# Performance work log

Measured on AMD Instinct MI355X. Metric: run time of the kernel, lower is better.

Reference implementation:

```python
import jax, jax.numpy as jnp
import numpy as np

N, E, H, ED, TD = 10000, 320000, 128, 64, 32

def _lin(x, w, b):
    return x @ w + b

def _ln(x, g, b, eps=1e-5):
    m = jnp.mean(x, axis=-1, keepdims=True)
    v = jnp.var(x, axis=-1, keepdims=True)
    return (x - m) * jax.lax.rsqrt(v + eps) * g + b

def _mlp(x, w1, b1, g, bt, w2, b2):
    y = jax.nn.silu(_ln(_lin(x, w1, b1), g, bt))
    return _lin(y, w2, b2)

def setup_inputs() -> dict:
    key = jax.random.key(0)
    ks = jax.random.split(key, 32)
    s = 0.02
    nrm = lambda k, shp: jax.random.normal(k, shp, jnp.float32) * s
    d = {}
    d['h'] = jax.random.normal(ks[0], (N, H), jnp.float32)
    d['edge_attr'] = jax.random.normal(ks[1], (E, ED), jnp.float32)
    d['edge_time_emb'] = jax.random.normal(ks[2], (E, TD), jnp.float32)
    d['edge_index'] = jax.random.randint(ks[3], (2, E), 0, N)
    # edge_emb + edge_norm
    d['w_ee'] = nrm(ks[4], (ED + TD, ED)); d['b_ee'] = jnp.zeros((ED,), jnp.float32)
    d['g_en'] = jnp.ones((ED + TD,), jnp.float32); d['bt_en'] = jnp.zeros((ED + TD,), jnp.float32)
    # node_linear / bond_linear
    d['w_nl'] = nrm(ks[5], (H, H)); d['b_nl'] = jnp.zeros((H,), jnp.float32)
    d['w_bl'] = nrm(ks[6], (ED, H)); d['b_bl'] = jnp.zeros((H,), jnp.float32)
    # bond_linear_left/right, node_linear_left/right
    d['w_bll'] = nrm(ks[7], (ED, H)); d['b_bll'] = jnp.zeros((H,), jnp.float32)
    d['w_blr'] = nrm(ks[8], (ED, H)); d['b_blr'] = jnp.zeros((H,), jnp.float32)
    d['w_nll'] = nrm(ks[9], (H, H)); d['b_nll'] = jnp.zeros((H,), jnp.float32)
    d['w_nlr'] = nrm(ks[10], (H, H)); d['b_nlr'] = jnp.zeros((H,), jnp.float32)
    # left / right MLPs: Linear(2H,H), LayerNorm(H), SiLU, Linear(H,H)
    d['mlpl_w1'] = nrm(ks[11], (2 * H, H)); d['mlpl_b1'] = jnp.zeros((H,), jnp.float32)
    d['mlpl_g'] = jnp.ones((H,), jnp.float32); d['mlpl_bt'] = jnp.zeros((H,), jnp.float32)
    d['mlpl_w2'] = nrm(ks[12], (H, H)); d['mlpl_b2'] = jnp.zeros((H,), jnp.float32)
    d['mlpr_w1'] = nrm(ks[13], (2 * H, H)); d['mlpr_b1'] = jnp.zeros((H,), jnp.float32)
    d['mlpr_g'] = jnp.ones((H,), jnp.float32); d['mlpr_bt'] = jnp.zeros((H,), jnp.float32)
    d['mlpr_w2'] = nrm(ks[14], (H, H)); d['mlpr_b2'] = jnp.zeros((H,), jnp.float32)
    # layer_norm(3H) + bond_out: Linear(3H,H), SiLU, Linear(H,ED)
    d['g_ln'] = jnp.ones((3 * H,), jnp.float32); d['bt_ln'] = jnp.zeros((3 * H,), jnp.float32)
    d['w_o1'] = nrm(ks[15], (3 * H, H)); d['b_o1'] = jnp.zeros((H,), jnp.float32)
    d['w_o2'] = nrm(ks[16], (H, ED)); d['b_o2'] = jnp.zeros((ED,), jnp.float32)
    return d

def reference(h, edge_attr, edge_time_emb, edge_index,
              w_ee, b_ee, g_en, bt_en, w_nl, b_nl, w_bl, b_bl,
              w_bll, b_bll, w_blr, b_blr, w_nll, b_nll, w_nlr, b_nlr,
              mlpl_w1, mlpl_b1, mlpl_g, mlpl_bt, mlpl_w2, mlpl_b2,
              mlpr_w1, mlpr_b1, mlpr_g, mlpr_bt, mlpr_w2, mlpr_b2,
              g_ln, bt_ln, w_o1, b_o1, w_o2, b_o2):
    src, dst = edge_index[0], edge_index[1]
    n = h.shape[0]
    # edge_attr = edge_emb(edge_norm(cat([edge_attr, edge_time_emb])))
    ea = _lin(_ln(jnp.concatenate([edge_attr, edge_time_emb], axis=-1), g_en, bt_en), w_ee, b_ee)
    # node linears applied per-node then gathered (same math as gather-then-linear)
    x_i = _lin(h, w_nll, b_nll)[src]            # [E, H]
    x_j = _lin(h, w_nlr, b_nlr)[dst]            # [E, H]
    edge_i = _lin(ea, w_bll, b_bll)             # [E, H]
    edge_j = _lin(ea, w_blr, b_blr)             # [E, H]
    inter_i = _mlp(jnp.concatenate([edge_i, x_i], axis=-1), mlpl_w1, mlpl_b1, mlpl_g, mlpl_bt, mlpl_w2, mlpl_b2)
    inter_j = _mlp(jnp.concatenate([edge_j, x_j], axis=-1), mlpr_w1, mlpr_b1, mlpr_g, mlpr_bt, mlpr_w2, mlpr_b2)
    # scatter_sum to nodes, then regather on the same index
    inter_i = jax.ops.segment_sum(inter_i, src, num_segments=n)[src]
    inter_j = jax.ops.segment_sum(inter_j, dst, num_segments=n)[dst]
    h_node = _lin(h, w_nl, b_nl)
    h_bond = jnp.concatenate([inter_i + inter_j, h_node[src] + h_node[dst], _lin(ea, w_bl, b_bl)], axis=-1)  # [E, 3H]
    h_bond = _ln(h_bond, g_ln, bt_ln)
    out = _lin(jax.nn.silu(_lin(h_bond, w_o1, b_o1)), w_o2, b_o2)  # [E, ED]
    return out
```

## Files before the change

kernel.cpp:

```cpp
#include <hip/hip_runtime.h>
#include <math.h>


using u16 = unsigned short;
using u32 = unsigned int;
typedef __attribute__((ext_vector_type(8))) short  short8;
typedef __attribute__((ext_vector_type(4))) float  f32x4;
typedef __attribute__((ext_vector_type(4))) u32    uint4v;
typedef __attribute__((ext_vector_type(2))) u32    uint2v;

constexpr int NN = 10000;
constexpr int EE = 320000;
constexpr int MAXDEG = 96;

__device__ __forceinline__ float b2f(u16 v) {
  return __builtin_bit_cast(float, (u32)v << 16);
}
__device__ __forceinline__ float b2f_lo(u32 v) {
  return __builtin_bit_cast(float, v << 16);
}
__device__ __forceinline__ float b2f_hi(u32 v) {
  return __builtin_bit_cast(float, v & 0xffff0000u);
}
__device__ __forceinline__ u32 cvtpk(float lo, float hi) {
  u32 r;
  asm("v_cvt_pk_bf16_f32 %0, %1, %2" : "=v"(r) : "v"(lo), "v"(hi));
  return r;
}
__device__ __forceinline__ u16 f2b(float f) {
  return (u16)cvtpk(f, f);
}
__device__ __forceinline__ uint2v pack4(f32x4 v) {
  uint2v r;
  r.x = cvtpk(v[0], v[1]);
  r.y = cvtpk(v[2], v[3]);
  return r;
}
__device__ __forceinline__ u32 addpk(u32 a, u32 b) {
  return cvtpk(b2f_lo(a) + b2f_lo(b), b2f_hi(a) + b2f_hi(b));
}
__device__ __forceinline__ float silu_f(float v) {
  return v * __builtin_amdgcn_rcpf(1.f + __expf(-v));
}
template<typename T>
__device__ __forceinline__ T ntld(const T* p) { return __builtin_nontemporal_load(p); }
template<typename T>
__device__ __forceinline__ void ntst(T* p, T v) { __builtin_nontemporal_store(v, p); }

struct Params {
  const void* h; const void* edge_attr; const void* te;
  const int* eidx;
  const int* flag;
  const u16 *b_ee, *g_en, *bt_en;
  const u16 *b_nl, *b_bl, *b_bll, *b_blr, *b_nll, *b_nlr;
  const u16 *l_b1, *l_g, *l_bt, *l_b2;
  const u16 *r_b1, *r_g, *r_bt, *r_b2;
  const u16 *g_ln, *bt_ln, *b_o1, *b_o2;
  const u16 *w_eeT, *w_blT, *w_bllT, *w_blrT, *w_nlT, *w_nllT, *w_nlrT;
  const u16 *l_w1T, *l_w2T, *r_w1T, *r_w2T, *o1T, *o2T;
  u16 *a_nll, *a_nlr, *tbl_i, *ea_ws;
  u32 *cnt0, *cnt1, *elist0, *elist1;
  u16 *accb_j;
  float *accf_i, *accf_j;
  u16 *inter0, *inter1;
  int amode;
  void *out;
};

__global__ __launch_bounds__(256) void k_sniff(const u16* p, int* flag)
{
  __shared__ int c;
  if (threadIdx.x == 0) c = 0;
  __syncthreads();
  u16 v = p[threadIdx.x * 2];
  int e = (v >> 7) & 0xff;
  if (e >= 100 && e <= 140) atomicAdd(&c, 1);
  __syncthreads();
  if (threadIdx.x == 0) *flag = (c >= 200) ? 1 : 0;
}

template<int K, int CT, int RT>
__device__ __forceinline__ void wave_gemm(const u16* A, int SA,
                                          const u16* __restrict__ BT,
                                          f32x4 (&acc)[RT][CT], int n0)
{
  const int lane = threadIdx.x & 63;
  const int quad = lane >> 4, l16 = lane & 15;
  constexpr int NKT = K / 32;
  constexpr int G = NKT < 4 ? NKT : 4;
#pragma unroll
  for (int g0 = 0; g0 < NKT; g0 += G) {
    short8 b[G][CT];
#pragma unroll
    for (int gg = 0; gg < G; ++gg)
#pragma unroll
      for (int c = 0; c < CT; ++c)
        b[gg][c] = *(const short8*)(BT + (size_t)(n0 + c * 16 + l16) * K +
                                    (g0 + gg) * 32 + quad * 8);
    __builtin_amdgcn_sched_barrier(0);
#pragma unroll
    for (int gg = 0; gg < G; ++gg) {
      const int k0 = (g0 + gg) * 32 + quad * 8;
#pragma unroll
      for (int rt = 0; rt < RT; ++rt) {
        short8 av = *(const short8*)(A + (rt * 16 + l16) * SA + k0);
#pragma unroll
        for (int c = 0; c < CT; ++c)
          acc[rt][c] = __builtin_amdgcn_mfma_f32_16x16x32_bf16(av, b[gg][c], acc[rt][c], 0, 0, 0);
      }
    }
  }
}

template<int CT, int RT, bool SILU>
__device__ __forceinline__ void epi_lds(f32x4 (&acc)[RT][CT], u16* O, int SO,
                                        int outc0, const u16* __restrict__ bias,
                                        int biasc0)
{
  const int lane = threadIdx.x & 63;
  const int quad = lane >> 4, l16 = lane & 15;
#pragma unroll
  for (int c = 0; c < CT; ++c) {
    float bv = b2f(bias[biasc0 + c * 16 + l16]);
#pragma unroll
    for (int rt = 0; rt < RT; ++rt) {
#pragma unroll
      for (int r = 0; r < 4; ++r) {
        float v = acc[rt][c][r] + bv;
        if (SILU) v = silu_f(v);
        O[(rt * 16 + quad * 4 + r) * SO + outc0 + c * 16 + l16] = f2b(v);
      }
    }
  }
}

template<int D, int ROWS, bool SILU>
__device__ __forceinline__ void ln_rows(u16* buf, int S,
                                        const u16* __restrict__ g,
                                        const u16* __restrict__ bt, float* red)
{
  constexpr int P = 256 / ROWS;
  constexpr int C = D / P;
  constexpr int NV = C / 8;
  const int t = threadIdx.x;
  const int row = t / P, p = t % P;
  u16* r = buf + row * S + p * C;
  uint4v vv[NV];
  float s = 0.f, ss = 0.f;
#pragma unroll
  for (int n = 0; n < NV; ++n) {
    vv[n] = *(const uint4v*)(r + n * 8);
#pragma unroll
    for (int q = 0; q < 4; ++q) {
      float lo = b2f_lo(vv[n][q]), hi = b2f_hi(vv[n][q]);
      s += lo + hi;
      ss += lo * lo + hi * hi;
    }
  }
  red[row * 2 * P + p] = s;
  red[row * 2 * P + P + p] = ss;
  __syncthreads();
  float S1 = 0.f, S2 = 0.f;
#pragma unroll
  for (int q = 0; q < P / 4; ++q) {
    f32x4 x = *(const f32x4*)&red[row * 2 * P + q * 4];
    f32x4 y = *(const f32x4*)&red[row * 2 * P + P + q * 4];
    S1 += x[0] + x[1] + x[2] + x[3];
    S2 += y[0] + y[1] + y[2] + y[3];
  }
  const float mean = S1 / (float)D;
  const float var  = S2 / (float)D - mean * mean;
  const float rstd = rsqrtf(var + 1e-5f);
#pragma unroll
  for (int n = 0; n < NV; ++n) {
    uint4v gv = *(const uint4v*)(g + p * C + n * 8);
    uint4v bv = *(const uint4v*)(bt + p * C + n * 8);
    uint4v ov;
#pragma unroll
    for (int q = 0; q < 4; ++q) {
      float lo = (b2f_lo(vv[n][q]) - mean) * rstd * b2f_lo(gv[q]) + b2f_lo(bv[q]);
      float hi = (b2f_hi(vv[n][q]) - mean) * rstd * b2f_hi(gv[q]) + b2f_hi(bv[q]);
      if (SILU) { lo = silu_f(lo); hi = silu_f(hi); }
      ov[q] = cvtpk(lo, hi);
    }
    *(uint4v*)(r + n * 8) = ov;
  }
  __syncthreads();
}

struct TDesc { const void* s; u16* d; int K; int N; };
struct TArgs { TDesc t[34]; const int* flag; };

__global__ __launch_bounds__(256) void k_transpose(TArgs a)
{
  const int flag = *a.flag;
  TDesc dsc = a.t[blockIdx.y];
  const int total = dsc.K * dsc.N;
  for (int i = blockIdx.x * 256 + threadIdx.x; i < total; i += gridDim.x * 256) {
    int n = i / dsc.K;
    int k = i - n * dsc.K;
    size_t si = (size_t)k * dsc.N + n;
    dsc.d[i] = flag ? ((const u16*)dsc.s)[si] : f2b(((const float*)dsc.s)[si]);
  }
}

__global__ __launch_bounds__(256) void k_hist(const int* eidx, u32* cnt0,
                                              u32* elist0, u32* cnt1, u32* elist1)
{
  int e = blockIdx.x * 256 + threadIdx.x;
  if (e >= EE) return;
  int n0 = eidx[e];
  u32 p0 = atomicAdd(&cnt0[n0], 1u);
  if (p0 < MAXDEG) elist0[(size_t)n0 * MAXDEG + p0] = (u32)e;
  int n1 = eidx[EE + e];
  u32 p1 = atomicAdd(&cnt1[n1], 1u);
  if (p1 < MAXDEG) elist1[(size_t)n1 * MAXDEG + p1] = (u32)e;
}

__global__ __launch_bounds__(256) void k_node(Params a)
{
  __shared__ __align__(16) u16 hs[64 * 136];
  const int tid = threadIdx.x, w = tid >> 6;
  const int n0 = blockIdx.x * 64;
  const int flag = *a.flag;
  if (flag) {
    for (int c = tid; c < 1024; c += 256) {
      int row = c >> 4, cc = c & 15;
      int node = n0 + row;
      uint4v v = {};
      if (node < NN) v = ntld((const uint4v*)((const u16*)a.h + (size_t)node * 128 + cc * 8));
      *(uint4v*)&hs[row * 136 + cc * 8] = v;
    }
  } else {
    for (int c = tid; c < 2048; c += 256) {
      int row = c >> 5, cc = c & 31;
      int node = n0 + row;
      uint2v pk = {};
      if (node < NN) {
        f32x4 fv = ntld((const f32x4*)((const float*)a.h + (size_t)node * 128 + cc * 4));
        pk = pack4(fv);
      }
      *(uint2v*)&hs[row * 136 + cc * 4] = pk;
    }
  }
  __syncthreads();
  const u16* wT[3] = { a.w_nllT, a.w_nlrT, a.w_nlT };
  const u16* bs[3] = { a.b_nll, a.b_nlr, a.b_nl };
  u16* os[3] = { a.a_nll, a.a_nlr, a.tbl_i + 128 };
  const int st[3] = { 128, 128, 256 };
  const int lane = tid & 63, quad = lane >> 4, l16 = lane & 15;
#pragma unroll 1
  for (int m = 0; m < 3; ++m) {
    f32x4 acc[4][2] = {};
    wave_gemm<128, 2, 4>(hs, 136, wT[m], acc, w * 32);
#pragma unroll
    for (int c = 0; c < 2; ++c) {
      int col = w * 32 + c * 16 + l16;
      float bv = b2f(bs[m][col]);
#pragma unroll
      for (int rt = 0; rt < 4; ++rt) {
#pragma unroll
        for (int r = 0; r < 4; ++r) {
          int node = n0 + rt * 16 + quad * 4 + r;
          if (node < NN) os[m][(size_t)node * st[m] + col] = f2b(acc[rt][c][r] + bv);
        }
      }
    }
  }
}

__global__ __launch_bounds__(256) void k_ea(Params a)
{
  __shared__ __align__(16) u16 u[64 * 104];
  __shared__ __align__(16) u16 eas[64 * 72];
  __shared__ float red[512];
  const int tid = threadIdx.x, w = tid >> 6;
  const int e0 = blockIdx.x * 64;
  const int flag = *a.flag;
  if (flag) {
    for (int c = tid; c < 512; c += 256) {
      int row = c >> 3, cc = c & 7;
      *(uint4v*)&u[row * 104 + cc * 8] =
          ntld((const uint4v*)((const u16*)a.edge_attr + (size_t)(e0 + row) * 64 + cc * 8));
    }
    {
      int row = tid >> 2, cc = tid & 3;
      *(uint4v*)&u[row * 104 + 64 + cc * 8] =
          ntld((const uint4v*)((const u16*)a.te + (size_t)(e0 + row) * 32 + cc * 8));
    }
  } else {
    for (int c = tid; c < 1024; c += 256) {
      int row = c >> 4, cc = c & 15;
      f32x4 fv = ntld((const f32x4*)((const float*)a.edge_attr + (size_t)(e0 + row) * 64 + cc * 4));
      *(uint2v*)&u[row * 104 + cc * 4] = pack4(fv);
    }
    for (int c = tid; c < 512; c += 256) {
      int row = c >> 3, cc = c & 7;
      f32x4 fv = ntld((const f32x4*)((const float*)a.te + (size_t)(e0 + row) * 32 + cc * 4));
      *(uint2v*)&u[row * 104 + 64 + cc * 4] = pack4(fv);
    }
  }
  __syncthreads();
  ln_rows<96, 64, false>(u, 104, a.g_en, a.bt_en, red);
  {
    f32x4 acc[4][1] = {};
    wave_gemm<96, 1, 4>(u, 104, a.w_eeT, acc, w * 16);
    epi_lds<1, 4, false>(acc, eas, 72, w * 16, a.b_ee, w * 16);
  }
  __syncthreads();
  for (int c = tid; c < 512; c += 256) {
    int row = c >> 3, cc = c & 7;
    *(uint4v*)(a.ea_ws + (size_t)(e0 + row) * 64 + cc * 8) =
        *(const uint4v*)&eas[row * 72 + cc * 8];
  }
}

template<bool ATOMIC>
__global__ __launch_bounds__(256, 4) void k_mlp(
    const u16* __restrict__ ea_ws, const int* __restrict__ eidx_side,
    const u16* __restrict__ an, const u16* __restrict__ wbT,
    const u16* __restrict__ bb, const u16* __restrict__ w1T,
    const u16* __restrict__ b1, const u16* __restrict__ gg,
    const u16* __restrict__ bt, const u16* __restrict__ w2T,
    const u16* __restrict__ b2, u16* __restrict__ inter,
    float* __restrict__ accf)
{
  __shared__ __align__(16) u16 u[64 * 264];
  __shared__ float red[512];
  __shared__ int sidx[64];
  const int tid = threadIdx.x, w = tid >> 6;
  const int e0 = blockIdx.x * 64;
  const int lane = tid & 63, quad = lane >> 4, l16 = lane & 15;

  if (tid < 64) sidx[tid] = eidx_side[e0 + tid];
  __syncthreads();
  for (int c = tid; c < 1024; c += 256) {
    int row = c >> 4, cc = c & 15;
    *(uint4v*)&u[row * 264 + 128 + cc * 8] =
        *(const uint4v*)(an + (size_t)sidx[row] * 128 + cc * 8);
  }
  {
    f32x4 acc[4][2] = {};
    wave_gemm<64, 2, 4>(ea_ws + (size_t)e0 * 64, 64, wbT, acc, w * 32);
    epi_lds<2, 4, false>(acc, u, 264, w * 32, bb, w * 32);
  }
  __syncthreads();
  {
    f32x4 acc[4][2] = {};
    wave_gemm<256, 2, 4>(u, 264, w1T, acc, w * 32);
    __syncthreads();
    epi_lds<2, 4, false>(acc, u, 264, w * 32, b1, w * 32);
  }
  __syncthreads();
  ln_rows<128, 64, true>(u, 264, gg, bt, red);
  {
    f32x4 acc[4][2] = {};
    wave_gemm<128, 2, 4>(u, 264, w2T, acc, w * 32);
    if (ATOMIC) {
#pragma unroll
      for (int c = 0; c < 2; ++c) {
        int col = w * 32 + c * 16 + l16;
        float bias = b2f(b2[col]);
#pragma unroll
        for (int rt = 0; rt < 4; ++rt)
#pragma unroll
          for (int r = 0; r < 4; ++r) {
            int row = rt * 16 + quad * 4 + r;
            unsafeAtomicAdd(accf + (size_t)sidx[row] * 128 + col,
                            acc[rt][c][r] + bias);
          }
      }
    } else {
      epi_lds<2, 4, false>(acc, u, 264, 128 + w * 32, b2, w * 32);
      __syncthreads();
      for (int c = tid; c < 1024; c += 256) {
        int row = c >> 4, cc = c & 15;
        ntst((uint4v*)(inter + (size_t)(e0 + row) * 128 + cc * 8),
             *(const uint4v*)&u[row * 264 + 128 + cc * 8]);
      }
    }
  }
}

__global__ __launch_bounds__(256) void k_nodesum(const u16* __restrict__ inter,
                                                 const u32* __restrict__ cnt,
                                                 const u32* __restrict__ elist,
                                                 u16* __restrict__ dst, int dstride)
{
  const int wv = (blockIdx.x * 256 + threadIdx.x) >> 6;
  const int lane = threadIdx.x & 63;
  if (wv >= NN) return;
  u32 deg = cnt[wv];
  if (deg > MAXDEG) deg = MAXDEG;
  const u32* el = elist + (size_t)wv * MAXDEG;
  float s0 = 0.f, s1 = 0.f;
  u32 d = 0;
  for (; d + 4 <= deg; d += 4) {
    uint4v ev = ntld((const uint4v*)(el + d));
    u32 v0 = ntld((const u32*)(inter + (size_t)ev[0] * 128 + lane * 2));
    u32 v1 = ntld((const u32*)(inter + (size_t)ev[1] * 128 + lane * 2));
    u32 v2 = ntld((const u32*)(inter + (size_t)ev[2] * 128 + lane * 2));
    u32 v3 = ntld((const u32*)(inter + (size_t)ev[3] * 128 + lane * 2));
    s0 += b2f_lo(v0) + b2f_lo(v1) + b2f_lo(v2) + b2f_lo(v3);
    s1 += b2f_hi(v0) + b2f_hi(v1) + b2f_hi(v2) + b2f_hi(v3);
  }
  for (; d < deg; ++d) {
    u32 e = el[d];
    u32 v = ntld((const u32*)(inter + (size_t)e * 128 + lane * 2));
    s0 += b2f_lo(v);
    s1 += b2f_hi(v);
  }
  *(u32*)(dst + (size_t)wv * dstride + lane * 2) = cvtpk(s0, s1);
}

__global__ __launch_bounds__(256, 4) void k_stage2(Params a)
{
  __shared__ __align__(16) u16 bond[32 * 392];
  __shared__ float red[512];
  __shared__ int sidx[2][32];
  const int tid = threadIdx.x, w = tid >> 6;
  const int e0 = blockIdx.x * 32;
  const int flag = *a.flag;
  const int lane = tid & 63, quad = lane >> 4, l16 = lane & 15;

  if (tid < 64) {
    int side = tid >> 5, i = tid & 31;
    sidx[side][i] = a.eidx[(size_t)side * EE + e0 + i];
  }
  __syncthreads();
  if (a.amode) {
    for (int c = tid; c < 1024; c += 256) {
      int row = c >> 5, cc = c & 31;
      const u16* ps = a.tbl_i + (size_t)sidx[0][row] * 256 + cc * 8;
      const u16* pp = (cc < 16)
          ? a.accb_j + (size_t)sidx[1][row] * 128 + cc * 8
          : a.tbl_i + (size_t)sidx[1][row] * 256 + cc * 8;
      uint4v vs = *(const uint4v*)ps;
      uint4v vp = *(const uint4v*)pp;
      uint4v ov;
#pragma unroll
      for (int q = 0; q < 4; ++q) ov[q] = addpk(vs[q], vp[q]);
      *(uint4v*)&bond[row * 392 + cc * 8] = ov;
    }
  } else {
    for (int c = tid; c < 1024; c += 256) {
      int row = c >> 5, cc = c & 31;
      f32x4 vi = *(const f32x4*)(a.accf_i + (size_t)sidx[0][row] * 128 + cc * 4);
      f32x4 vj = *(const f32x4*)(a.accf_j + (size_t)sidx[1][row] * 128 + cc * 4);
      f32x4 sm = vi + vj;
      *(uint2v*)&bond[row * 392 + cc * 4] = pack4(sm);
    }
    for (int c = tid; c < 512; c += 256) {
      int row = c >> 4, cc = c & 15;
      uint4v hs = *(const uint4v*)(a.tbl_i + (size_t)sidx[0][row] * 256 + 128 + cc * 8);
      uint4v hd = *(const uint4v*)(a.tbl_i + (size_t)sidx[1][row] * 256 + 128 + cc * 8);
      uint4v ov;
#pragma unroll
      for (int q = 0; q < 4; ++q) ov[q] = addpk(hs[q], hd[q]);
      *(uint4v*)&bond[row * 392 + 128 + cc * 8] = ov;
    }
  }
  {
    f32x4 acc[2][2] = {};
    wave_gemm<64, 2, 2>(a.ea_ws + (size_t)e0 * 64, 64, a.w_blT, acc, w * 32);
    epi_lds<2, 2, false>(acc, bond, 392, 256 + w * 32, a.b_bl, w * 32);
  }
  __syncthreads();
  ln_rows<384, 32, false>(bond, 392, a.g_ln, a.bt_ln, red);
  {
    f32x4 acc[2][2] = {};
    wave_gemm<384, 2, 2>(bond, 392, a.o1T, acc, w * 32);
    __syncthreads();
    epi_lds<2, 2, true>(acc, bond, 392, w * 32, a.b_o1, w * 32);
  }
  __syncthreads();
  {
    f32x4 acc[2][1] = {};
    wave_gemm<128, 1, 2>(bond, 392, a.o2T, acc, w * 16);
    if (flag) {
      epi_lds<1, 2, false>(acc, bond, 392, 128 + w * 16, a.b_o2, w * 16);
      __syncthreads();
      for (int c = tid; c < 256; c += 256) {
        int row = c >> 3, cc = c & 7;
        ntst((uint4v*)((u16*)a.out + (size_t)(e0 + row) * 64 + cc * 8),
             *(const uint4v*)&bond[row * 392 + 128 + cc * 8]);
      }
    } else {
      float bvv = b2f(a.b_o2[w * 16 + l16]);
#pragma unroll
      for (int rt = 0; rt < 2; ++rt)
#pragma unroll
        for (int r = 0; r < 4; ++r) {
          int row = rt * 16 + quad * 4 + r;
          ((float*)((char*)bond + (size_t)row * 784 + 272))[w * 16 + l16] =
              acc[rt][0][r] + bvv;
        }
      __syncthreads();
      for (int c = tid; c < 512; c += 256) {
        int row = c >> 4, cc = c & 15;
        f32x4 v = *(const f32x4*)((char*)bond + (size_t)row * 784 + 272 + cc * 16);
        ntst((f32x4*)((float*)a.out + (size_t)(e0 + row) * 64 + cc * 4), v);
      }
    }
  }
}

extern "C" void kernel_launch(void* const* d_in, const int* in_sizes, int n_in,
                              void* d_out, int out_size, void* d_ws, size_t ws_size,
                              hipStream_t stream)
{
  char* ws = (char*)d_ws;

  const size_t O_EET  = 0;
  const size_t O_BLT  = 12288;
  const size_t O_BLLT = O_BLT  + 16384;
  const size_t O_BLRT = O_BLLT + 16384;
  const size_t O_NLT  = O_BLRT + 16384;
  const size_t O_NLLT = O_NLT  + 32768;
  const size_t O_NLRT = O_NLLT + 32768;
  const size_t O_LW1T = O_NLRT + 32768;
  const size_t O_LW2T = O_LW1T + 65536;
  const size_t O_RW1T = O_LW2T + 32768;
  const size_t O_RW2T = O_RW1T + 65536;
  const size_t O_O1T  = O_RW2T + 32768;
  const size_t O_O2T  = O_O1T  + 98304;
  const size_t PRM    = O_O2T  + 16384;
  const size_t FLAG   = PRM + 6016;
  const size_t A_NLL  = PRM + 6144;
  const size_t A_NLR  = A_NLL + 2560000;
  const size_t TBL_I  = A_NLR + 2560000;
  const size_t EA     = TBL_I + 5120000;
  const size_t TAIL   = EA + 40960000;
  const size_t ACCF_I = TAIL;
  const size_t ACCF_J = TAIL + 5120000;
  const size_t NEED_ATOM = TAIL + 10240000;
  const size_t CNT0   = TAIL;
  const size_t CNT1   = TAIL + 40960;
  const size_t EL0    = TAIL + 81920;
  const size_t EL1    = EL0 + 3840000;
  const size_t ACCB_J = EL1 + 3840000;
  const size_t INTER0 = ACCB_J + 2560000;
  const size_t NEED_CSR = INTER0 + 81920000;
  if (ws_size < NEED_ATOM) return;
  const int amode = (ws_size >= NEED_CSR) ? 1 : 0;

  const size_t pOff[21] = { 0, 128, 320, 512, 768, 1024, 1280, 1536, 1792,
                            2048, 2304, 2560, 2816, 3072, 3328, 3584, 3840,
                            4096, 4864, 5632, 5888 };
  const int   pIdx[21] = { 5, 6, 7, 9, 11, 13, 15, 17, 19,
                           21, 22, 23, 25, 27, 28, 29, 31,
                           32, 33, 35, 37 };
  const int   pLen[21] = { 64, 96, 96, 128, 128, 128, 128, 128, 128,
                           128, 128, 128, 128, 128, 128, 128, 128,
                           384, 384, 128, 64 };
  auto P = [&](int slot) { return (const u16*)(ws + PRM + pOff[slot]); };

  Params a;
  a.h = d_in[0]; a.edge_attr = d_in[1]; a.te = d_in[2];
  a.eidx = (const int*)d_in[3];
  a.flag = (const int*)(ws + FLAG);
  a.b_ee = P(0); a.g_en = P(1); a.bt_en = P(2);
  a.b_nl = P(3); a.b_bl = P(4); a.b_bll = P(5); a.b_blr = P(6);
  a.b_nll = P(7); a.b_nlr = P(8);
  a.l_b1 = P(9); a.l_g = P(10); a.l_bt = P(11); a.l_b2 = P(12);
  a.r_b1 = P(13); a.r_g = P(14); a.r_bt = P(15); a.r_b2 = P(16);
  a.g_ln = P(17); a.bt_ln = P(18); a.b_o1 = P(19); a.b_o2 = P(20);
  a.w_eeT = (const u16*)(ws + O_EET);   a.w_blT  = (const u16*)(ws + O_BLT);
  a.w_bllT = (const u16*)(ws + O_BLLT); a.w_blrT = (const u16*)(ws + O_BLRT);
  a.w_nlT = (const u16*)(ws + O_NLT);   a.w_nllT = (const u16*)(ws + O_NLLT);
  a.w_nlrT = (const u16*)(ws + O_NLRT);
  a.l_w1T = (const u16*)(ws + O_LW1T);  a.l_w2T = (const u16*)(ws + O_LW2T);
  a.r_w1T = (const u16*)(ws + O_RW1T);  a.r_w2T = (const u16*)(ws + O_RW2T);
  a.o1T = (const u16*)(ws + O_O1T);     a.o2T = (const u16*)(ws + O_O2T);
  a.a_nll = (u16*)(ws + A_NLL); a.a_nlr = (u16*)(ws + A_NLR);
  a.tbl_i = (u16*)(ws + TBL_I); a.ea_ws = (u16*)(ws + EA);
  a.cnt0 = (u32*)(ws + CNT0); a.cnt1 = (u32*)(ws + CNT1);
  a.elist0 = (u32*)(ws + EL0); a.elist1 = (u32*)(ws + EL1);
  a.accb_j = (u16*)(ws + ACCB_J);
  a.accf_i = (float*)(ws + ACCF_I); a.accf_j = (float*)(ws + ACCF_J);
  a.inter0 = (u16*)(ws + INTER0); a.inter1 = (u16*)(ws + INTER0);
  a.amode = amode;
  a.out = d_out;

  TArgs ta;
  ta.flag = (const int*)(ws + FLAG);
  ta.t[0]  = { d_in[4],  (u16*)(ws + O_EET),  96, 64 };
  ta.t[1]  = { d_in[10], (u16*)(ws + O_BLT),  64, 128 };
  ta.t[2]  = { d_in[12], (u16*)(ws + O_BLLT), 64, 128 };
  ta.t[3]  = { d_in[14], (u16*)(ws + O_BLRT), 64, 128 };
  ta.t[4]  = { d_in[8],  (u16*)(ws + O_NLT),  128, 128 };
  ta.t[5]  = { d_in[16], (u16*)(ws + O_NLLT), 128, 128 };
  ta.t[6]  = { d_in[18], (u16*)(ws + O_NLRT), 128, 128 };
  ta.t[7]  = { d_in[20], (u16*)(ws + O_LW1T), 256, 128 };
  ta.t[8]  = { d_in[24], (u16*)(ws + O_LW2T), 128, 128 };
  ta.t[9]  = { d_in[26], (u16*)(ws + O_RW1T), 256, 128 };
  ta.t[10] = { d_in[30], (u16*)(ws + O_RW2T), 128, 128 };
  ta.t[11] = { d_in[34], (u16*)(ws + O_O1T),  384, 128 };
  ta.t[12] = { d_in[36], (u16*)(ws + O_O2T),  128, 64 };
  for (int s = 0; s < 21; ++s)
    ta.t[13 + s] = { d_in[pIdx[s]], (u16*)(ws + PRM + pOff[s]), 1, pLen[s] };

  k_sniff<<<1, 256, 0, stream>>>((const u16*)d_in[1], (int*)(ws + FLAG));
  if (amode) hipMemsetAsync(ws + CNT0, 0, 81920, stream);
  else       hipMemsetAsync(ws + ACCF_I, 0, 10240000, stream);
  k_transpose<<<dim3(16, 34), 256, 0, stream>>>(ta);
  if (amode)
    k_hist<<<(EE + 255) / 256, 256, 0, stream>>>(a.eidx, a.cnt0, a.elist0, a.cnt1, a.elist1);
  k_node<<<(NN + 63) / 64, 256, 0, stream>>>(a);
  k_ea<<<EE / 64, 256, 0, stream>>>(a);

  if (amode) {
    k_mlp<false><<<EE / 64, 256, 0, stream>>>(a.ea_ws, a.eidx, a.a_nll, a.w_bllT,
        a.b_bll, a.l_w1T, a.l_b1, a.l_g, a.l_bt, a.l_w2T, a.l_b2, a.inter0, nullptr);
    k_nodesum<<<(NN * 64 + 255) / 256, 256, 0, stream>>>(a.inter0, a.cnt0, a.elist0,
        a.tbl_i, 256);
    k_mlp<false><<<EE / 64, 256, 0, stream>>>(a.ea_ws, a.eidx + EE, a.a_nlr, a.w_blrT,
        a.b_blr, a.r_w1T, a.r_b1, a.r_g, a.r_bt, a.r_w2T, a.r_b2, a.inter1, nullptr);
    k_nodesum<<<(NN * 64 + 255) / 256, 256, 0, stream>>>(a.inter1, a.cnt1, a.elist1,
        a.accb_j, 128);
  } else {
    k_mlp<true><<<EE / 64, 256, 0, stream>>>(a.ea_ws, a.eidx, a.a_nll, a.w_bllT,
        a.b_bll, a.l_w1T, a.l_b1, a.l_g, a.l_bt, a.l_w2T, a.l_b2, nullptr, a.accf_i);
    k_mlp<true><<<EE / 64, 256, 0, stream>>>(a.ea_ws, a.eidx + EE, a.a_nlr, a.w_blrT,
        a.b_blr, a.r_w1T, a.r_b1, a.r_g, a.r_bt, a.r_w2T, a.r_b2, nullptr, a.accf_j);
  }
  k_stage2<<<EE / 32, 256, 0, stream>>>(a);
}
```

Before: 770.0 us.

## Halve edge tiles and use two waves per block in MLP and stage2

The edge-MLP and stage2 kernels now use 128-thread blocks over half as many edges (32 and 16 rows), and each wave covers 64 output columns instead of 32. This cuts LDS use per block and raises the block count, with the aim of better occupancy and more concurrency. The wave GEMM also drops the grouped B-prefetch and its scheduling barrier in favour of a plain per-k-step load loop. In exchange, B-fragment reuse across rows drops, since each B load now feeds only one or two row tiles, so global weight traffic per edge rises.

After: 979.8 us. +27.3%, slower.

```diff
diff --git a/kernel.cpp b/kernel.cpp
--- a/kernel.cpp
+++ b/kernel.cpp
@@ -86,28 +86,19 @@
 {
   const int lane = threadIdx.x & 63;
   const int quad = lane >> 4, l16 = lane & 15;
-  constexpr int NKT = K / 32;
-  constexpr int G = NKT < 4 ? NKT : 4;
-#pragma unroll
-  for (int g0 = 0; g0 < NKT; g0 += G) {
-    short8 b[G][CT];
-#pragma unroll
-    for (int gg = 0; gg < G; ++gg)
+#pragma unroll
+  for (int kt = 0; kt < K / 32; ++kt) {
+    const int k0 = kt * 32 + quad * 8;
+    short8 b[CT];
+#pragma unroll
+    for (int c = 0; c < CT; ++c)
+      b[c] = *(const short8*)(BT + (size_t)(n0 + c * 16 + l16) * K + k0);
+#pragma unroll
+    for (int rt = 0; rt < RT; ++rt) {
+      short8 av = *(const short8*)(A + (rt * 16 + l16) * SA + k0);
 #pragma unroll
       for (int c = 0; c < CT; ++c)
-        b[gg][c] = *(const short8*)(BT + (size_t)(n0 + c * 16 + l16) * K +
-                                    (g0 + gg) * 32 + quad * 8);
-    __builtin_amdgcn_sched_barrier(0);
-#pragma unroll
-    for (int gg = 0; gg < G; ++gg) {
-      const int k0 = (g0 + gg) * 32 + quad * 8;
-#pragma unroll
-      for (int rt = 0; rt < RT; ++rt) {
-        short8 av = *(const short8*)(A + (rt * 16 + l16) * SA + k0);
-#pragma unroll
-        for (int c = 0; c < CT; ++c)
-          acc[rt][c] = __builtin_amdgcn_mfma_f32_16x16x32_bf16(av, b[gg][c], acc[rt][c], 0, 0, 0);
-      }
+        acc[rt][c] = __builtin_amdgcn_mfma_f32_16x16x32_bf16(av, b[c], acc[rt][c], 0, 0, 0);
     }
   }
 }
@@ -134,12 +125,12 @@
   }
 }
 
-template<int D, int ROWS, bool SILU>
+template<int D, int ROWS, bool SILU, int NT = 256>
 __device__ __forceinline__ void ln_rows(u16* buf, int S,
                                         const u16* __restrict__ g,
                                         const u16* __restrict__ bt, float* red)
 {
-  constexpr int P = 256 / ROWS;
+  constexpr int P = NT / ROWS;
   constexpr int C = D / P;
   constexpr int NV = C / 8;
   const int t = threadIdx.x;
@@ -301,7 +292,7 @@
     }
   }
   __syncthreads();
-  ln_rows<96, 64, false>(u, 104, a.g_en, a.bt_en, red);
+  ln_rows<96, 64, false, 256>(u, 104, a.g_en, a.bt_en, red);
   {
     f32x4 acc[4][1] = {};
     wave_gemm<96, 1, 4>(u, 104, a.w_eeT, acc, w * 16);
@@ -316,7 +307,7 @@
 }
 
 template<bool ATOMIC>
-__global__ __launch_bounds__(256, 4) void k_mlp(
+__global__ __launch_bounds__(128, 4) void k_mlp(
     const u16* __restrict__ ea_ws, const int* __restrict__ eidx_side,
     const u16* __restrict__ an, const u16* __restrict__ wbT,
     const u16* __restrict__ bb, const u16* __restrict__ w1T,
@@ -325,44 +316,44 @@
     const u16* __restrict__ b2, u16* __restrict__ inter,
     float* __restrict__ accf)
 {
-  __shared__ __align__(16) u16 u[64 * 264];
-  __shared__ float red[512];
-  __shared__ int sidx[64];
+  __shared__ __align__(16) u16 u[32 * 264];
+  __shared__ float red[256];
+  __shared__ int sidx[32];
   const int tid = threadIdx.x, w = tid >> 6;
-  const int e0 = blockIdx.x * 64;
+  const int e0 = blockIdx.x * 32;
   const int lane = tid & 63, quad = lane >> 4, l16 = lane & 15;
 
-  if (tid < 64) sidx[tid] = eidx_side[e0 + tid];
-  __syncthreads();
-  for (int c = tid; c < 1024; c += 256) {
+  if (tid < 32) sidx[tid] = eidx_side[e0 + tid];
+  __syncthreads();
+  for (int c = tid; c < 512; c += 128) {
     int row = c >> 4, cc = c & 15;
     *(uint4v*)&u[row * 264 + 128 + cc * 8] =
         *(const uint4v*)(an + (size_t)sidx[row] * 128 + cc * 8);
   }
   {
-    f32x4 acc[4][2] = {};
-    wave_gemm<64, 2, 4>(ea_ws + (size_t)e0 * 64, 64, wbT, acc, w * 32);
-    epi_lds<2, 4, false>(acc, u, 264, w * 32, bb, w * 32);
+    f32x4 acc[2][4] = {};
+    wave_gemm<64, 4, 2>(ea_ws + (size_t)e0 * 64, 64, wbT, acc, w * 64);
+    epi_lds<4, 2, false>(acc, u, 264, w * 64, bb, w * 64);
   }
   __syncthreads();
   {
-    f32x4 acc[4][2] = {};
-    wave_gemm<256, 2, 4>(u, 264, w1T, acc, w * 32);
+    f32x4 acc[2][4] = {};
+    wave_gemm<256, 4, 2>(u, 264, w1T, acc, w * 64);
     __syncthreads();
-    epi_lds<2, 4, false>(acc, u, 264, w * 32, b1, w * 32);
-  }
-  __syncthreads();
-  ln_rows<128, 64, true>(u, 264, gg, bt, red);
+    epi_lds<4, 2, false>(acc, u, 264, w * 64, b1, w * 64);
+  }
+  __syncthreads();
+  ln_rows<128, 32, true, 128>(u, 264, gg, bt, red);
   {
-    f32x4 acc[4][2] = {};
-    wave_gemm<128, 2, 4>(u, 264, w2T, acc, w * 32);
+    f32x4 acc[2][4] = {};
+    wave_gemm<128, 4, 2>(u, 264, w2T, acc, w * 64);
     if (ATOMIC) {
 #pragma unroll
-      for (int c = 0; c < 2; ++c) {
-        int col = w * 32 + c * 16 + l16;
+      for (int c = 0; c < 4; ++c) {
+        int col = w * 64 + c * 16 + l16;
         float bias = b2f(b2[col]);
 #pragma unroll
-        for (int rt = 0; rt < 4; ++rt)
+        for (int rt = 0; rt < 2; ++rt)
 #pragma unroll
           for (int r = 0; r < 4; ++r) {
             int row = rt * 16 + quad * 4 + r;
@@ -371,9 +362,9 @@
           }
       }
     } else {
-      epi_lds<2, 4, false>(acc, u, 264, 128 + w * 32, b2, w * 32);
+      epi_lds<4, 2, false>(acc, u, 264, 128 + w * 64, b2, w * 64);
       __syncthreads();
-      for (int c = tid; c < 1024; c += 256) {
+      for (int c = tid; c < 512; c += 128) {
         int row = c >> 4, cc = c & 15;
         ntst((uint4v*)(inter + (size_t)(e0 + row) * 128 + cc * 8),
              *(const uint4v*)&u[row * 264 + 128 + cc * 8]);
@@ -413,23 +404,23 @@
   *(u32*)(dst + (size_t)wv * dstride + lane * 2) = cvtpk(s0, s1);
 }
 
-__global__ __launch_bounds__(256, 4) void k_stage2(Params a)
-{
-  __shared__ __align__(16) u16 bond[32 * 392];
-  __shared__ float red[512];
-  __shared__ int sidx[2][32];
+__global__ __launch_bounds__(128, 4) void k_stage2(Params a)
+{
+  __shared__ __align__(16) u16 bond[16 * 392];
+  __shared__ float red[256];
+  __shared__ int sidx[2][16];
   const int tid = threadIdx.x, w = tid >> 6;
-  const int e0 = blockIdx.x * 32;
+  const int e0 = blockIdx.x * 16;
   const int flag = *a.flag;
   const int lane = tid & 63, quad = lane >> 4, l16 = lane & 15;
 
-  if (tid < 64) {
-    int side = tid >> 5, i = tid & 31;
+  if (tid < 32) {
+    int side = tid >> 4, i = tid & 15;
     sidx[side][i] = a.eidx[(size_t)side * EE + e0 + i];
   }
   __syncthreads();
   if (a.amode) {
-    for (int c = tid; c < 1024; c += 256) {
+    for (int c = tid; c < 512; c += 128) {
       int row = c >> 5, cc = c & 31;
       const u16* ps = a.tbl_i + (size_t)sidx[0][row] * 256 + cc * 8;
       const u16* pp = (cc < 16)
@@ -443,14 +434,14 @@
       *(uint4v*)&bond[row * 392 + cc * 8] = ov;
     }
   } else {
-    for (int c = tid; c < 1024; c += 256) {
+    for (int c = tid; c < 512; c += 128) {
       int row = c >> 5, cc = c & 31;
       f32x4 vi = *(const f32x4*)(a.accf_i + (size_t)sidx[0][row] * 128 + cc * 4);
       f32x4 vj = *(const f32x4*)(a.accf_j + (size_t)sidx[1][row] * 128 + cc * 4);
       f32x4 sm = vi + vj;
       *(uint2v*)&bond[row * 392 + cc * 4] = pack4(sm);
     }
-    for (int c = tid; c < 512; c += 256) {
+    for (int c = tid; c < 256; c += 128) {
       int row = c >> 4, cc = c & 15;
       uint4v hs = *(const uint4v*)(a.tbl_i + (size_t)sidx[0][row] * 256 + 128 + cc * 8);
       uint4v hd = *(const uint4v*)(a.tbl_i + (size_t)sidx[1][row] * 256 + 128 + cc * 8);
@@ -461,42 +452,44 @@
     }
   }
   {
-    f32x4 acc[2][2] = {};
-    wave_gemm<64, 2, 2>(a.ea_ws + (size_t)e0 * 64, 64, a.w_blT, acc, w * 32);
-    epi_lds<2, 2, false>(acc, bond, 392, 256 + w * 32, a.b_bl, w * 32);
-  }
-  __syncthreads();
-  ln_rows<384, 32, false>(bond, 392, a.g_ln, a.bt_ln, red);
+    f32x4 acc[1][4] = {};
+    wave_gemm<64, 4, 1>(a.ea_ws + (size_t)e0 * 64, 64, a.w_blT, acc, w * 64);
+    epi_lds<4, 1, false>(acc, bond, 392, 256 + w * 64, a.b_bl, w * 64);
+  }
+  __syncthreads();
+  ln_rows<384, 16, false, 128>(bond, 392, a.g_ln, a.bt_ln, red);
   {
-    f32x4 acc[2][2] = {};
-    wave_gemm<384, 2, 2>(bond, 392, a.o1T, acc, w * 32);
+    f32x4 acc[1][4] = {};
+    wave_gemm<384, 4, 1>(bond, 392, a.o1T, acc, w * 64);
     __syncthreads();
-    epi_lds<2, 2, true>(acc, bond, 392, w * 32, a.b_o1, w * 32);
+    epi_lds<4, 1, true>(acc, bond, 392, w * 64, a.b_o1, w * 64);
   }
   __syncthreads();
   {
-    f32x4 acc[2][1] = {};
-    wave_gemm<128, 1, 2>(bond, 392, a.o2T, acc, w * 16);
+    f32x4 acc[1][2] = {};
+    wave_gemm<128, 2, 1>(bond, 392, a.o2T, acc, w * 32);
     if (flag) {
-      epi_lds<1, 2, false>(acc, bond, 392, 128 + w * 16, a.b_o2, w * 16);
+      epi_lds<2, 1, false>(acc, bond, 392, 128 + w * 32, a.b_o2, w * 32);
       __syncthreads();
-      for (int c = tid; c < 256; c += 256) {
+      for (int c = tid; c < 128; c += 128) {
         int row = c >> 3, cc = c & 7;
         ntst((uint4v*)((u16*)a.out + (size_t)(e0 + row) * 64 + cc * 8),
              *(const uint4v*)&bond[row * 392 + 128 + cc * 8]);
       }
     } else {
-      float bvv = b2f(a.b_o2[w * 16 + l16]);
-#pragma unroll
-      for (int rt = 0; rt < 2; ++rt)
+#pragma unroll
+      for (int c = 0; c < 2; ++c) {
+        int col = w * 32 + c * 16 + l16;
+        float bvv = b2f(a.b_o2[col]);
 #pragma unroll
         for (int r = 0; r < 4; ++r) {
-          int row = rt * 16 + quad * 4 + r;
-          ((float*)((char*)bond + (size_t)row * 784 + 272))[w * 16 + l16] =
-              acc[rt][0][r] + bvv;
+          int row = quad * 4 + r;
+          ((float*)((char*)bond + (size_t)row * 784 + 272))[col] =
+              acc[0][c][r] + bvv;
         }
+      }
       __syncthreads();
-      for (int c = tid; c < 512; c += 256) {
+      for (int c = tid; c < 256; c += 128) {
         int row = c >> 4, cc = c & 15;
         f32x4 v = *(const f32x4*)((char*)bond + (size_t)row * 784 + 272 + cc * 16);
         ntst((f32x4*)((float*)a.out + (size_t)(e0 + row) * 64 + cc * 4), v);
@@ -610,19 +603,19 @@
   k_ea<<<EE / 64, 256, 0, stream>>>(a);
 
   if (amode) {
-    k_mlp<false><<<EE / 64, 256, 0, stream>>>(a.ea_ws, a.eidx, a.a_nll, a.w_bllT,
+    k_mlp<false><<<EE / 32, 128, 0, stream>>>(a.ea_ws, a.eidx, a.a_nll, a.w_bllT,
         a.b_bll, a.l_w1T, a.l_b1, a.l_g, a.l_bt, a.l_w2T, a.l_b2, a.inter0, nullptr);
     k_nodesum<<<(NN * 64 + 255) / 256, 256, 0, stream>>>(a.inter0, a.cnt0, a.elist0,
         a.tbl_i, 256);
-    k_mlp<false><<<EE / 64, 256, 0, stream>>>(a.ea_ws, a.eidx + EE, a.a_nlr, a.w_blrT,
+    k_mlp<false><<<EE / 32, 128, 0, stream>>>(a.ea_ws, a.eidx + EE, a.a_nlr, a.w_blrT,
         a.b_blr, a.r_w1T, a.r_b1, a.r_g, a.r_bt, a.r_w2T, a.r_b2, a.inter1, nullptr);
     k_nodesum<<<(NN * 64 + 255) / 256, 256, 0, stream>>>(a.inter1, a.cnt1, a.elist1,
         a.accb_j, 128);
   } else {
-    k_mlp<true><<<EE / 64, 256, 0, stream>>>(a.ea_ws, a.eidx, a.a_nll, a.w_bllT,
+    k_mlp<true><<<EE / 32, 128, 0, stream>>>(a.ea_ws, a.eidx, a.a_nll, a.w_bllT,
         a.b_bll, a.l_w1T, a.l_b1, a.l_g, a.l_bt, a.l_w2T, a.l_b2, nullptr, a.accf_i);
-    k_mlp<true><<<EE / 64, 256, 0, stream>>>(a.ea_ws, a.eidx + EE, a.a_nlr, a.w_blrT,
+    k_mlp<true><<<EE / 32, 128, 0, stream>>>(a.ea_ws, a.eidx + EE, a.a_nlr, a.w_blrT,
         a.b_blr, a.r_w1T, a.r_b1, a.r_g, a.r_bt, a.r_w2T, a.r_b2, nullptr, a.accf_j);
   }
-  k_stage2<<<EE / 32, 256, 0, stream>>>(a);
-}
+  k_stage2<<<EE / 16, 128, 0, stream>>>(a);
+}
```
